# Optimization experiments

Measured on AMD Instinct MI355X. Metric: run time of the kernel, lower is better.

The kernel has to match this reference:

```python
import jax, jax.numpy as jnp
import numpy as np

D_MODEL = 1024
D_STATE = 16
D_CONV = 4
EXPAND = 2
D_INNER = EXPAND * D_MODEL          # 2048
DT_RANK = (D_MODEL + 15) // 16      # 64
EPS = 1e-5
BATCH, SEQ = 2, 1024


def setup_inputs() -> dict:
    key = jax.random.key(0)
    ks = jax.random.split(key, 10)
    s = 0.02
    x = jax.random.normal(ks[0], (BATCH, SEQ, D_MODEL), jnp.float32)
    norm_w = jnp.ones((D_MODEL,), jnp.float32)
    in_proj_w = jax.random.normal(ks[1], (2 * D_INNER, D_MODEL), jnp.float32) * s
    conv_w = jax.random.normal(ks[2], (D_INNER, D_CONV), jnp.float32) * 0.2
    conv_b = jnp.zeros((D_INNER,), jnp.float32)
    x_proj_w = jax.random.normal(ks[3], (DT_RANK + 2 * D_STATE, D_INNER), jnp.float32) * s
    dt_proj_w = jax.random.normal(ks[4], (D_INNER, DT_RANK), jnp.float32) * s
    dt_proj_b = jnp.full((D_INNER,), -2.0, jnp.float32)  # softplus(-2) ~ 0.127, realistic dt init
    # S4D-real init: A[d, n] = n+1  => A_log = log(1..N)
    A_log = jnp.log(jnp.broadcast_to(jnp.arange(1, D_STATE + 1, dtype=jnp.float32), (D_INNER, D_STATE)))
    D = jnp.ones((D_INNER,), jnp.float32)
    out_proj_w = jax.random.normal(ks[5], (D_MODEL, D_INNER), jnp.float32) * s
    return dict(x=x, norm_w=norm_w, in_proj_w=in_proj_w, conv_w=conv_w, conv_b=conv_b,
                x_proj_w=x_proj_w, dt_proj_w=dt_proj_w, dt_proj_b=dt_proj_b,
                A_log=A_log, D=D, out_proj_w=out_proj_w)


def _mamba_forward(x, norm_w, in_proj_w, conv_w, conv_b, x_proj_w,
                   dt_proj_w, dt_proj_b, A_log, D, out_proj_w):
    # Block: residual = x ; h = RMSNorm(residual) ; out = Mamba(h)
    residual = x
    h = x * jax.lax.rsqrt(jnp.mean(x * x, axis=-1, keepdims=True) + EPS) * norm_w

    # in_proj -> split into (xc, z), each [B, L, D_INNER]
    xz = jnp.einsum('bld,ed->ble', h, in_proj_w)
    xc, z = jnp.split(xz, 2, axis=-1)

    # causal depthwise conv1d (kernel D_CONV) + SiLU
    xp = jnp.pad(xc, ((0, 0), (D_CONV - 1, 0), (0, 0)))
    conv = conv_b
    for k in range(D_CONV):  # tiny fixed loop over kernel taps
        conv = conv + conv_w[:, k] * xp[:, k:k + SEQ, :]
    xs = jax.nn.silu(conv)  # [B, L, D_INNER]

    # x_proj -> dt, B_t, C_t
    x_dbl = jnp.einsum('bld,ed->ble', xs, x_proj_w)
    dt_r = x_dbl[..., :DT_RANK]
    B_t = x_dbl[..., DT_RANK:DT_RANK + D_STATE]           # [B, L, N]
    C_t = x_dbl[..., DT_RANK + D_STATE:]                  # [B, L, N]
    dt = jax.nn.softplus(jnp.einsum('blr,dr->bld', dt_r, dt_proj_w) + dt_proj_b)  # [B, L, D_INNER]

    # selective scan: h_t = exp(dt*A) h_{t-1} + dt * B_t * u_t ; y_t = C_t . h_t + D u_t
    A = -jnp.exp(A_log)                                   # [D_INNER, N]
    deltaA = jnp.exp(dt[..., None] * A)                   # [B, L, D_INNER, N]
    deltaBu = (dt * xs)[..., None] * B_t[:, :, None, :]   # [B, L, D_INNER, N]

    def combine(e1, e2):
        a1, b1 = e1
        a2, b2 = e2
        return a1 * a2, a2 * b1 + b2

    _, hstates = jax.lax.associative_scan(combine, (deltaA, deltaBu), axis=1)
    y = jnp.einsum('bldn,bln->bld', hstates, C_t) + D * xs
    y = y * jax.nn.silu(z)
    out = jnp.einsum('bld,ed->ble', y, out_proj_w)

    # MambaBlock: y = mixer_out + residual
    return out + residual


def reference(x, norm_w, in_proj_w, conv_w, conv_b, x_proj_w,
              dt_proj_w, dt_proj_b, A_log, D, out_proj_w):
    return _mamba_forward(x, norm_w, in_proj_w, conv_w, conv_b, x_proj_w,
                          dt_proj_w, dt_proj_b, A_log, D, out_proj_w)
```

## Files before the change

### kernel.cpp

```cpp
#include <hip/hip_runtime.h>
#include <hip/hip_bf16.h>


#define BATCH 2
#define SEQ 1024
#define DMODEL 1024
#define DINNER 2048
#define DTRANK 64
#define DSTATE 16
#define NROWS (BATCH * SEQ)
#define NC 32
#define CL (SEQ / NC)
#define NSPLIT 8
#define KCH (DINNER / NSPLIT)

typedef __bf16 bf16_t;
typedef __bf16 bf16x4 __attribute__((ext_vector_type(4)));
typedef __bf16 bf16x8 __attribute__((ext_vector_type(8)));
typedef float f32x4 __attribute__((ext_vector_type(4)));

__global__ __launch_bounds__(256) void k_prep(
    const float* __restrict__ x, const float* __restrict__ w,
    bf16_t* __restrict__ h,
    const float* __restrict__ s0, bf16_t* __restrict__ d0,
    const float* __restrict__ s1, bf16_t* __restrict__ d1,
    const float* __restrict__ s2, bf16_t* __restrict__ d2)
{
    const int tid = threadIdx.x;
    if (blockIdx.x < NROWS) {
        const int row = blockIdx.x;
        const float* xr = x + (size_t)row * DMODEL;
        float4 xv = *(const float4*)(xr + tid * 4);
        float s = xv.x * xv.x + xv.y * xv.y + xv.z * xv.z + xv.w * xv.w;
#pragma unroll
        for (int m = 1; m <= 32; m <<= 1) s += __shfl_xor(s, m, 64);
        __shared__ float red[4];
        if ((tid & 63) == 0) red[tid >> 6] = s;
        __syncthreads();
        float tot = red[0] + red[1] + red[2] + red[3];
        float scale = rsqrtf(tot * (1.0f / DMODEL) + 1e-5f);
        float4 wv = *(const float4*)(w + tid * 4);
        bf16x4 hv;
        hv.x = (bf16_t)(xv.x * scale * wv.x);
        hv.y = (bf16_t)(xv.y * scale * wv.y);
        hv.z = (bf16_t)(xv.z * scale * wv.z);
        hv.w = (bf16_t)(xv.w * scale * wv.w);
        *(bf16x4*)(h + (size_t)row * DMODEL + tid * 4) = hv;
        return;
    }
    const int i = (blockIdx.x - NROWS) * 256 + tid;
    const float* src; bf16_t* dst; int off;
    if (i < 1048576) { src = s0; dst = d0; off = i; }
    else if (i < 1048576 + 524288) { src = s1; dst = d1; off = i - 1048576; }
    else { src = s2; dst = d2; off = i - 1048576 - 524288; }
    float4 v = *(const float4*)(src + (size_t)off * 4);
    bf16x4 o;
    o.x = (bf16_t)v.x; o.y = (bf16_t)v.y; o.z = (bf16_t)v.z; o.w = (bf16_t)v.w;
    *(bf16x4*)(dst + (size_t)off * 4) = o;
}

template <int BM, int BN, bool BF16_OUT>
__global__ __launch_bounds__(256) void k_gemm_db(
    const bf16_t* __restrict__ A,
    const bf16_t* __restrict__ W,
    void* __restrict__ Cv, int ldc,
    const float* __restrict__ resid,
    int K)
{
    constexpr int NGA = BM / 32;
    constexpr int NGB = BN / 32;
    constexpr int MF = BM / 32;
    constexpr int NF = BN / 32;

    __shared__ __align__(16) bf16_t lA[2][BM * 64];
    __shared__ __align__(16) bf16_t lB[2][BN * 64];

    const int tid = threadIdx.x;
    const int wave = tid >> 6;
    const int lane = tid & 63;
    const int m0 = blockIdx.x * BM;
    const int n0 = blockIdx.y * BN;
    const int wm = (wave >> 1) * (BM / 2);
    const int wn = (wave & 1) * (BN / 2);
    const int fr = lane & 15;
    const int fg = lane >> 4;

    int a_row[NGA], a_col[NGA], b_row[NGB], b_col[NGB];
#pragma unroll
    for (int g = 0; g < NGA; ++g) {
        const int gi = g * 256 + tid;
        a_row[g] = gi >> 3;
        a_col[g] = (gi & 7) ^ (a_row[g] & 7);
    }
#pragma unroll
    for (int g = 0; g < NGB; ++g) {
        const int gi = g * 256 + tid;
        b_row[g] = gi >> 3;
        b_col[g] = (gi & 7) ^ (b_row[g] & 7);
    }

    f32x4 acc[MF][NF] = {};
    bf16x8 ra[NGA], rb[NGB];

#pragma unroll
    for (int g = 0; g < NGA; ++g)
        ra[g] = *(const bf16x8*)(A + (size_t)(m0 + a_row[g]) * K + a_col[g] * 8);
#pragma unroll
    for (int g = 0; g < NGB; ++g)
        rb[g] = *(const bf16x8*)(W + (size_t)(n0 + b_row[g]) * K + b_col[g] * 8);
#pragma unroll
    for (int g = 0; g < NGA; ++g)
        *(bf16x8*)(lA[0] + (size_t)(g * 256 + tid) * 8) = ra[g];
#pragma unroll
    for (int g = 0; g < NGB; ++g)
        *(bf16x8*)(lB[0] + (size_t)(g * 256 + tid) * 8) = rb[g];

    for (int k0 = 0; k0 < K; k0 += 64) {
        const int p = (k0 >> 6) & 1;
        const bool more = (k0 + 64) < K;
        __syncthreads();
        if (more) {
#pragma unroll
            for (int g = 0; g < NGA; ++g)
                ra[g] = *(const bf16x8*)(A + (size_t)(m0 + a_row[g]) * K + (k0 + 64) + a_col[g] * 8);
#pragma unroll
            for (int g = 0; g < NGB; ++g)
                rb[g] = *(const bf16x8*)(W + (size_t)(n0 + b_row[g]) * K + (k0 + 64) + b_col[g] * 8);
        }
#pragma unroll
        for (int s = 0; s < 2; ++s) {
            bf16x8 af[MF], bf[NF];
#pragma unroll
            for (int i = 0; i < MF; ++i) {
                const int rr = wm + i * 16 + fr;
                af[i] = *(const bf16x8*)(lA[p] + (size_t)(rr * 8 + ((s * 4 + fg) ^ (rr & 7))) * 8);
            }
#pragma unroll
            for (int j = 0; j < NF; ++j) {
                const int rr = wn + j * 16 + fr;
                bf[j] = *(const bf16x8*)(lB[p] + (size_t)(rr * 8 + ((s * 4 + fg) ^ (rr & 7))) * 8);
            }
#pragma unroll
            for (int i = 0; i < MF; ++i)
#pragma unroll
                for (int j = 0; j < NF; ++j)
                    acc[i][j] = __builtin_amdgcn_mfma_f32_16x16x32_bf16(
                        af[i], bf[j], acc[i][j], 0, 0, 0);
        }
        if (more) {
#pragma unroll
            for (int g = 0; g < NGA; ++g)
                *(bf16x8*)(lA[p ^ 1] + (size_t)(g * 256 + tid) * 8) = ra[g];
#pragma unroll
            for (int g = 0; g < NGB; ++g)
                *(bf16x8*)(lB[p ^ 1] + (size_t)(g * 256 + tid) * 8) = rb[g];
        }
    }

#pragma unroll
    for (int i = 0; i < MF; ++i) {
        const int rbase = m0 + wm + i * 16 + (lane >> 4) * 4;
#pragma unroll
        for (int rr = 0; rr < 4; ++rr) {
            const int row = rbase + rr;
            if (BF16_OUT) {
                bf16_t* cr = (bf16_t*)Cv + (size_t)row * ldc;
#pragma unroll
                for (int j = 0; j < NF; ++j)
                    cr[n0 + wn + j * 16 + fr] = (bf16_t)acc[i][j][rr];
            } else {
                float* cr = (float*)Cv + (size_t)row * ldc;
                const float* ar = resid + (size_t)row * ldc;
#pragma unroll
                for (int j = 0; j < NF; ++j) {
                    const int col = n0 + wn + j * 16 + fr;
                    cr[col] = acc[i][j][rr] + ar[col];
                }
            }
        }
    }
}

#define XBK 16
__global__ __launch_bounds__(256) void k_gemm_xproj(
    const bf16_t* __restrict__ xz,
    const float* __restrict__ cw,
    const float* __restrict__ cb,
    const float* __restrict__ W,
    float* __restrict__ part,
    bf16_t* __restrict__ xsout)
{
    __shared__ __align__(16) float As[XBK][64 + 4];
    __shared__ __align__(16) float Ws[XBK][96 + 4];
    __shared__ float cwL[KCH * 4];
    __shared__ float cbL[KCH];
    const int tid = threadIdx.x;
    const int m0 = blockIdx.x * 64;
    const int kbase = blockIdx.y * KCH;
    const int lrow = tid >> 2;
    const int lk4 = (tid & 3) << 2;
    const int tm = tid >> 4;
    const int tn = tid & 15;

    {
        float4 v = *(const float4*)(cw + (size_t)kbase * 4 + tid * 4);
        *(float4*)&cwL[tid * 4] = v;
        cbL[tid] = cb[kbase + tid];
    }
    __syncthreads();

    float acc[4][6] = {};

    for (int k0 = 0; k0 < KCH; k0 += XBK) {
        {
            const int eloc = k0 + lk4;
            const int l = m0 + lrow;
            const int lloc = l & (SEQ - 1);
            float s0 = cbL[eloc], s1 = cbL[eloc + 1],
                  s2 = cbL[eloc + 2], s3 = cbL[eloc + 3];
#pragma unroll
            for (int kk = 0; kk < 4; ++kk) {
                const int ll = lloc - 3 + kk;
                if (ll >= 0) {
                    bf16x4 xv = *(const bf16x4*)(xz + (size_t)(l - 3 + kk) * (2 * DINNER)
                                                 + kbase + eloc);
                    s0 = fmaf(cwL[(eloc + 0) * 4 + kk], (float)xv.x, s0);
                    s1 = fmaf(cwL[(eloc + 1) * 4 + kk], (float)xv.y, s1);
                    s2 = fmaf(cwL[(eloc + 2) * 4 + kk], (float)xv.z, s2);
                    s3 = fmaf(cwL[(eloc + 3) * 4 + kk], (float)xv.w, s3);
                }
            }
            s0 = s0 / (1.0f + __expf(-s0));
            s1 = s1 / (1.0f + __expf(-s1));
            s2 = s2 / (1.0f + __expf(-s2));
            s3 = s3 / (1.0f + __expf(-s3));
            As[lk4 + 0][lrow] = s0;
            As[lk4 + 1][lrow] = s1;
            As[lk4 + 2][lrow] = s2;
            As[lk4 + 3][lrow] = s3;
            bf16x4 o;
            o.x = (bf16_t)s0; o.y = (bf16_t)s1; o.z = (bf16_t)s2; o.w = (bf16_t)s3;
            *(bf16x4*)(xsout + (size_t)l * DINNER + kbase + eloc) = o;
        }
        {
            float4 v = *(const float4*)(W + (size_t)lrow * DINNER + kbase + k0 + lk4);
            Ws[lk4 + 0][lrow] = v.x;
            Ws[lk4 + 1][lrow] = v.y;
            Ws[lk4 + 2][lrow] = v.z;
            Ws[lk4 + 3][lrow] = v.w;
        }
        if (tid < 128) {
            float4 v = *(const float4*)(W + (size_t)(64 + lrow) * DINNER + kbase + k0 + lk4);
            Ws[lk4 + 0][64 + lrow] = v.x;
            Ws[lk4 + 1][64 + lrow] = v.y;
            Ws[lk4 + 2][64 + lrow] = v.z;
            Ws[lk4 + 3][64 + lrow] = v.w;
        }
        __syncthreads();
#pragma unroll
        for (int kk = 0; kk < XBK; ++kk) {
            float4 av = *(const float4*)&As[kk][tm * 4];
            float a4[4] = {av.x, av.y, av.z, av.w};
#pragma unroll
            for (int j = 0; j < 6; ++j) {
                const float wv = Ws[kk][tn * 6 + j];
#pragma unroll
                for (int i = 0; i < 4; ++i) acc[i][j] = fmaf(a4[i], wv, acc[i][j]);
            }
        }
        __syncthreads();
    }
    float* pb = part + (size_t)blockIdx.y * NROWS * 96;
#pragma unroll
    for (int i = 0; i < 4; ++i) {
        float* pr = pb + (size_t)(m0 + tm * 4 + i) * 96 + tn * 6;
#pragma unroll
        for (int j = 0; j < 6; ++j) pr[j] = acc[i][j];
    }
}

__global__ __launch_bounds__(256) void k_xproj_reduce(
    const float* __restrict__ part, float* __restrict__ xdbl,
    bf16_t* __restrict__ dtr)
{
    const int idx = blockIdx.x * 256 + threadIdx.x;
    if (idx >= NROWS * 24) return;
    const int row = idx / 24;
    const int c4 = (idx % 24) * 4;
    f32x4 s = {0.f, 0.f, 0.f, 0.f};
#pragma unroll
    for (int p = 0; p < NSPLIT; ++p)
        s += *(const f32x4*)(part + (size_t)p * NROWS * 96 + (size_t)row * 96 + c4);
    *(f32x4*)(xdbl + (size_t)row * 96 + c4) = s;
    if (c4 < 64) {
        bf16x4 o;
        o.x = (bf16_t)s.x; o.y = (bf16_t)s.y; o.z = (bf16_t)s.z; o.w = (bf16_t)s.w;
        *(bf16x4*)(dtr + (size_t)row * 64 + c4) = o;
    }
}

__global__ __launch_bounds__(256) void k_scan_sum(
    const bf16_t* __restrict__ dtlin, const float* __restrict__ dtb,
    const bf16_t* __restrict__ xs, const float* __restrict__ xdbl,
    float* __restrict__ Qpb, float* __restrict__ sloc)
{
    const int tid = threadIdx.x;
    const int g = blockIdx.x & 7;
    const int c = (blockIdx.x >> 3) & (NC - 1);
    const int b = blockIdx.x >> 8;
    const int d0 = g * 256;
    const int d = d0 + tid;

    __shared__ __align__(16) bf16_t sDT[CL * 256];
    __shared__ __align__(16) bf16_t sXS[CL * 256];
    __shared__ float sB[CL * 16];
    {
        const int t = tid >> 4, n = tid & 15;
#pragma unroll
        for (int tt = 0; tt < CL; tt += 16)
            sB[(t + tt) * 16 + n] =
                xdbl[(size_t)(b * SEQ + c * CL + t + tt) * 96 + 64 + n];
    }
#pragma unroll
    for (int i = 0; i < 4; ++i) {
        const int gi = i * 256 + tid;
        const int t = gi >> 5;
        const int c8 = (gi & 31) * 8;
        const size_t ga = (size_t)(b * SEQ + c * CL + t) * DINNER + d0 + c8;
        *(bf16x8*)(sDT + t * 256 + c8) = *(const bf16x8*)(dtlin + ga);
        *(bf16x8*)(sXS + t * 256 + c8) = *(const bf16x8*)(xs + ga);
    }

    float st[16];
#pragma unroll
    for (int n = 0; n < 16; ++n) st[n] = 0.0f;
    float P = 1.0f;
    const float bias = dtb[d];
    __syncthreads();

    for (int t = 0; t < CL; ++t) {
        const float dlv = (float)sDT[t * 256 + tid] + bias;
        const float dtv = (dlv > 20.0f) ? dlv : __logf(1.0f + __expf(dlv));
        const float du = dtv * (float)sXS[t * 256 + tid];
        const float q = __expf(-dtv);
        P *= q;
        float a = q;
#pragma unroll
        for (int n4 = 0; n4 < 4; ++n4) {
            const f32x4 Bv = *(const f32x4*)&sB[t * 16 + n4 * 4];
#pragma unroll
            for (int j = 0; j < 4; ++j) {
                st[n4 * 4 + j] = a * st[n4 * 4 + j] + du * Bv[j];
                a *= q;
            }
        }
    }
    Qpb[(size_t)(b * NC + c) * DINNER + d] = P;
#pragma unroll
    for (int n = 0; n < 16; ++n)
        sloc[((size_t)((b * NC + c) * 16 + n)) * DINNER + d] = st[n];
}

__global__ __launch_bounds__(256) void k_scan_combine(
    const float* __restrict__ Qpb, const float* __restrict__ sloc,
    float* __restrict__ hinit)
{
    const int tid = threadIdx.x;
    const int g = blockIdx.x & 7;
    const int n = (blockIdx.x >> 3) & 15;
    const int b = blockIdx.x >> 7;
    const int d = g * 256 + tid;
    float h = 0.0f;
    for (int c = 0; c < NC; ++c) {
        const size_t i16 = ((size_t)((b * NC + c) * 16 + n)) * DINNER + d;
        hinit[i16] = h;
        const float Q = Qpb[(size_t)(b * NC + c) * DINNER + d];
        float Qn = Q;
        for (int i = 0; i < n; ++i) Qn *= Q;
        h = Qn * h + sloc[i16];
    }
}

__global__ __launch_bounds__(256) void k_scan_out(
    const bf16_t* __restrict__ dtlin, const float* __restrict__ dtb,
    const bf16_t* __restrict__ xs, const float* __restrict__ xdbl,
    const bf16_t* __restrict__ xz, const float* __restrict__ Dp,
    const float* __restrict__ hinit,
    bf16_t* __restrict__ yg)
{
    const int tid = threadIdx.x;
    const int g = blockIdx.x & 7;
    const int c = (blockIdx.x >> 3) & (NC - 1);
    const int b = blockIdx.x >> 8;
    const int d0 = g * 256;
    const int d = d0 + tid;

    __shared__ __align__(16) bf16_t sDT[CL * 256];
    __shared__ __align__(16) bf16_t sXS[CL * 256];
    __shared__ __align__(16) bf16_t sZ[CL * 256];
    __shared__ float sB[CL * 16];
    __shared__ float sC[CL * 16];
    {
        const int t = tid >> 4, n = tid & 15;
#pragma unroll
        for (int tt = 0; tt < CL; tt += 16) {
            const size_t base = (size_t)(b * SEQ + c * CL + t + tt) * 96;
            sB[(t + tt) * 16 + n] = xdbl[base + 64 + n];
            sC[(t + tt) * 16 + n] = xdbl[base + 80 + n];
        }
    }
#pragma unroll
    for (int i = 0; i < 4; ++i) {
        const int gi = i * 256 + tid;
        const int t = gi >> 5;
        const int c8 = (gi & 31) * 8;
        const int row = b * SEQ + c * CL + t;
        const size_t ga = (size_t)row * DINNER + d0 + c8;
        *(bf16x8*)(sDT + t * 256 + c8) = *(const bf16x8*)(dtlin + ga);
        *(bf16x8*)(sXS + t * 256 + c8) = *(const bf16x8*)(xs + ga);
        *(bf16x8*)(sZ + t * 256 + c8) =
            *(const bf16x8*)(xz + (size_t)row * (2 * DINNER) + DINNER + d0 + c8);
    }

    float st[16];
#pragma unroll
    for (int n = 0; n < 16; ++n)
        st[n] = hinit[((size_t)((b * NC + c) * 16 + n)) * DINNER + d];
    const float bias = dtb[d];
    const float Dd = Dp[d];
    __syncthreads();

    for (int t = 0; t < CL; ++t) {
        const float dlv = (float)sDT[t * 256 + tid] + bias;
        const float dtv = (dlv > 20.0f) ? dlv : __logf(1.0f + __expf(dlv));
        const float xv = (float)sXS[t * 256 + tid];
        const float du = dtv * xv;
        const float q = __expf(-dtv);
        float a = q;
        float part = 0.0f;
#pragma unroll
        for (int n4 = 0; n4 < 4; ++n4) {
            const f32x4 Bv = *(const f32x4*)&sB[t * 16 + n4 * 4];
            const f32x4 Cw = *(const f32x4*)&sC[t * 16 + n4 * 4];
#pragma unroll
            for (int j = 0; j < 4; ++j) {
                const int n = n4 * 4 + j;
                st[n] = a * st[n] + du * Bv[j];
                part = fmaf(st[n], Cw[j], part);
                a *= q;
            }
        }
        const float zv = (float)sZ[t * 256 + tid];
        const float sig = 1.0f / (1.0f + __expf(-zv));
        yg[(size_t)(b * SEQ + c * CL + t) * DINNER + d] =
            (bf16_t)((part + Dd * xv) * (zv * sig));
    }
}

extern "C" void kernel_launch(void* const* d_in, const int* in_sizes, int n_in,
                              void* d_out, int out_size, void* d_ws, size_t ws_size,
                              hipStream_t stream) {
    const float* x = (const float*)d_in[0];
    const float* norm_w = (const float*)d_in[1];
    const float* in_proj_w = (const float*)d_in[2];
    const float* conv_w = (const float*)d_in[3];
    const float* conv_b = (const float*)d_in[4];
    const float* x_proj_w = (const float*)d_in[5];
    const float* dt_proj_w = (const float*)d_in[6];
    const float* dt_proj_b = (const float*)d_in[7];
    const float* Dp = (const float*)d_in[9];
    const float* out_proj_w = (const float*)d_in[10];
    float* out = (float*)d_out;

    char* ws = (char*)d_ws;
    bf16_t* xz    = (bf16_t*)(ws);
    bf16_t* xsb   = (bf16_t*)(ws + 16777216);
    float*  xdbl  = (float*) (ws + 25165824);
    bf16_t* dtl   = (bf16_t*)(ws + 25952256);
    float*  sloc  = (float*) (ws + 34340864);
    float*  Qpb   = (float*) (ws + 42729472);
    float*  hinit = (float*) (ws + 43253760);
    bf16_t* ygb   = (bf16_t*)(ws + 51642368);
    bf16_t* hb    = (bf16_t*)(ws + 60030976);
    bf16_t* inw   = (bf16_t*)(ws + 64225280);
    bf16_t* outw  = (bf16_t*)(ws + 72613888);
    bf16_t* dtw   = (bf16_t*)(ws + 76808192);
    bf16_t* dtr   = (bf16_t*)(ws + 77070336);
    float*  xpart = (float*) (ws + 77332480);

    k_prep<<<NROWS + 6272, 256, 0, stream>>>(x, norm_w, hb,
                                             in_proj_w, inw,
                                             out_proj_w, outw,
                                             dt_proj_w, dtw);

    {
        dim3 g(NROWS / 128, (2 * DINNER) / 128);
        k_gemm_db<128, 128, true><<<g, 256, 0, stream>>>(hb, inw, xz, 2 * DINNER,
                                                         nullptr, DMODEL);
    }

    {
        dim3 g(NROWS / 64, NSPLIT);
        k_gemm_xproj<<<g, 256, 0, stream>>>(xz, conv_w, conv_b, x_proj_w,
                                            xpart, xsb);
    }
    k_xproj_reduce<<<(NROWS * 24 + 255) / 256, 256, 0, stream>>>(xpart, xdbl, dtr);

    {
        dim3 g(NROWS / 64, DINNER / 128);
        k_gemm_db<64, 128, true><<<g, 256, 0, stream>>>(dtr, dtw, dtl, DINNER,
                                                        nullptr, DTRANK);
    }

    k_scan_sum<<<BATCH * NC * 8, 256, 0, stream>>>(dtl, dt_proj_b, xsb, xdbl,
                                                   Qpb, sloc);
    k_scan_combine<<<BATCH * DSTATE * 8, 256, 0, stream>>>(Qpb, sloc, hinit);
    k_scan_out<<<BATCH * NC * 8, 256, 0, stream>>>(dtl, dt_proj_b, xsb, xdbl,
                                                   xz, Dp, hinit, ygb);

    {
        dim3 g(NROWS / 64, DMODEL / 64);
        k_gemm_db<64, 64, false><<<g, 256, 0, stream>>>(ygb, outw, out, DMODEL,
                                                        x, DINNER);
    }
}
```

Baseline: 238.5 us.

## Double-buffer xproj GEMM shared tiles and halve row tile to 32

The fused conv+SiLU+x_proj GEMM now uses a 32-row tile instead of 64, doubling the grid, and double-buffers the A/W shared-memory tiles. Global loads for the next K step are issued before the current step's FMAs and written to the alternate buffer afterwards, so one barrier per step is dropped. Each thread now computes a 2x6 accumulator with vectorized float2 LDS reads. The aim is more parallelism and latency hiding, at the cost of more redundant W loads across blocks and lower arithmetic intensity per thread.

```diff
diff --git a/kernel.cpp b/kernel.cpp
--- a/kernel.cpp
+++ b/kernel.cpp
@@ -15,6 +15,7 @@
 #define KCH (DINNER / NSPLIT)
 
 typedef __bf16 bf16_t;
+typedef __bf16 bf16x2 __attribute__((ext_vector_type(2)));
 typedef __bf16 bf16x4 __attribute__((ext_vector_type(4)));
 typedef __bf16 bf16x8 __attribute__((ext_vector_type(8)));
 typedef float f32x4 __attribute__((ext_vector_type(4)));
@@ -190,90 +191,116 @@
     float* __restrict__ part,
     bf16_t* __restrict__ xsout)
 {
-    __shared__ __align__(16) float As[XBK][64 + 4];
-    __shared__ __align__(16) float Ws[XBK][96 + 4];
+    __shared__ __align__(16) float As[2][XBK][36];
+    __shared__ __align__(16) float Ws[2][XBK][100];
     __shared__ float cwL[KCH * 4];
     __shared__ float cbL[KCH];
     const int tid = threadIdx.x;
-    const int m0 = blockIdx.x * 64;
+    const int m0 = blockIdx.x * 32;
     const int kbase = blockIdx.y * KCH;
-    const int lrow = tid >> 2;
-    const int lk4 = (tid & 3) << 2;
+
+    const int ar = tid >> 3;
+    const int ac = (tid & 7) << 1;
+    const int wr = tid >> 2;
+    const int wk = (tid & 3) << 2;
     const int tm = tid >> 4;
     const int tn = tid & 15;
+
+    const int l = m0 + ar;
+    const int lloc = l & (SEQ - 1);
 
     {
         float4 v = *(const float4*)(cw + (size_t)kbase * 4 + tid * 4);
         *(float4*)&cwL[tid * 4] = v;
         cbL[tid] = cb[kbase + tid];
     }
+
+    auto stage_load = [&](int kq, bf16x2 (&xv)[4], float4& wv0, float4& wv1) {
+#pragma unroll
+        for (int kk = 0; kk < 4; ++kk) {
+            bf16x2 z = {};
+            xv[kk] = z;
+            if (lloc - 3 + kk >= 0)
+                xv[kk] = *(const bf16x2*)(xz + (size_t)(l - 3 + kk) * (2 * DINNER)
+                                          + kbase + kq + ac);
+        }
+        wv0 = *(const float4*)(W + (size_t)wr * DINNER + kbase + kq + wk);
+        if (tid < 128)
+            wv1 = *(const float4*)(W + (size_t)(64 + wr) * DINNER + kbase + kq + wk);
+    };
+
+    auto stage_write = [&](int kq, int pbuf, const bf16x2 (&xv)[4],
+                           const float4& wv0, const float4& wv1) {
+        const int e = kq + ac;
+        float s0 = cbL[e], s1 = cbL[e + 1];
+#pragma unroll
+        for (int kk = 0; kk < 4; ++kk) {
+            s0 = fmaf(cwL[(e + 0) * 4 + kk], (float)xv[kk].x, s0);
+            s1 = fmaf(cwL[(e + 1) * 4 + kk], (float)xv[kk].y, s1);
+        }
+        s0 = s0 / (1.0f + __expf(-s0));
+        s1 = s1 / (1.0f + __expf(-s1));
+        As[pbuf][ac + 0][ar] = s0;
+        As[pbuf][ac + 1][ar] = s1;
+        bf16x2 o;
+        o.x = (bf16_t)s0; o.y = (bf16_t)s1;
+        *(bf16x2*)(xsout + (size_t)l * DINNER + kbase + e) = o;
+        Ws[pbuf][wk + 0][wr] = wv0.x;
+        Ws[pbuf][wk + 1][wr] = wv0.y;
+        Ws[pbuf][wk + 2][wr] = wv0.z;
+        Ws[pbuf][wk + 3][wr] = wv0.w;
+        if (tid < 128) {
+            Ws[pbuf][wk + 0][64 + wr] = wv1.x;
+            Ws[pbuf][wk + 1][64 + wr] = wv1.y;
+            Ws[pbuf][wk + 2][64 + wr] = wv1.z;
+            Ws[pbuf][wk + 3][64 + wr] = wv1.w;
+        }
+    };
+
     __syncthreads();
 
-    float acc[4][6] = {};
-
-    for (int k0 = 0; k0 < KCH; k0 += XBK) {
-        {
-            const int eloc = k0 + lk4;
-            const int l = m0 + lrow;
-            const int lloc = l & (SEQ - 1);
-            float s0 = cbL[eloc], s1 = cbL[eloc + 1],
-                  s2 = cbL[eloc + 2], s3 = cbL[eloc + 3];
-#pragma unroll
-            for (int kk = 0; kk < 4; ++kk) {
-                const int ll = lloc - 3 + kk;
-                if (ll >= 0) {
-                    bf16x4 xv = *(const bf16x4*)(xz + (size_t)(l - 3 + kk) * (2 * DINNER)
-                                                 + kbase + eloc);
-                    s0 = fmaf(cwL[(eloc + 0) * 4 + kk], (float)xv.x, s0);
-                    s1 = fmaf(cwL[(eloc + 1) * 4 + kk], (float)xv.y, s1);
-                    s2 = fmaf(cwL[(eloc + 2) * 4 + kk], (float)xv.z, s2);
-                    s3 = fmaf(cwL[(eloc + 3) * 4 + kk], (float)xv.w, s3);
-                }
-            }
-            s0 = s0 / (1.0f + __expf(-s0));
-            s1 = s1 / (1.0f + __expf(-s1));
-            s2 = s2 / (1.0f + __expf(-s2));
-            s3 = s3 / (1.0f + __expf(-s3));
-            As[lk4 + 0][lrow] = s0;
-            As[lk4 + 1][lrow] = s1;
-            As[lk4 + 2][lrow] = s2;
-            As[lk4 + 3][lrow] = s3;
-            bf16x4 o;
-            o.x = (bf16_t)s0; o.y = (bf16_t)s1; o.z = (bf16_t)s2; o.w = (bf16_t)s3;
-            *(bf16x4*)(xsout + (size_t)l * DINNER + kbase + eloc) = o;
-        }
-        {
-            float4 v = *(const float4*)(W + (size_t)lrow * DINNER + kbase + k0 + lk4);
-            Ws[lk4 + 0][lrow] = v.x;
-            Ws[lk4 + 1][lrow] = v.y;
-            Ws[lk4 + 2][lrow] = v.z;
-            Ws[lk4 + 3][lrow] = v.w;
-        }
-        if (tid < 128) {
-            float4 v = *(const float4*)(W + (size_t)(64 + lrow) * DINNER + kbase + k0 + lk4);
-            Ws[lk4 + 0][64 + lrow] = v.x;
-            Ws[lk4 + 1][64 + lrow] = v.y;
-            Ws[lk4 + 2][64 + lrow] = v.z;
-            Ws[lk4 + 3][64 + lrow] = v.w;
-        }
+    {
+        bf16x2 xv[4]; float4 wv0 = {}, wv1 = {};
+        stage_load(0, xv, wv0, wv1);
+        stage_write(0, 0, xv, wv0, wv1);
+    }
+
+    float acc[2][6] = {};
+    constexpr int NSTEP = KCH / XBK;
+
+    for (int ks = 0; ks < NSTEP; ++ks) {
+        const int p = ks & 1;
         __syncthreads();
+        const bool more = (ks + 1) < NSTEP;
+        bf16x2 xv[4]; float4 wv0 = {}, wv1 = {};
+        if (more) stage_load((ks + 1) * XBK, xv, wv0, wv1);
+
 #pragma unroll
         for (int kk = 0; kk < XBK; ++kk) {
-            float4 av = *(const float4*)&As[kk][tm * 4];
-            float a4[4] = {av.x, av.y, av.z, av.w};
-#pragma unroll
-            for (int j = 0; j < 6; ++j) {
-                const float wv = Ws[kk][tn * 6 + j];
-#pragma unroll
-                for (int i = 0; i < 4; ++i) acc[i][j] = fmaf(a4[i], wv, acc[i][j]);
-            }
-        }
-        __syncthreads();
-    }
+            const float2 av  = *(const float2*)&As[p][kk][tm * 2];
+            const float2 w01 = *(const float2*)&Ws[p][kk][tn * 6 + 0];
+            const float2 w23 = *(const float2*)&Ws[p][kk][tn * 6 + 2];
+            const float2 w45 = *(const float2*)&Ws[p][kk][tn * 6 + 4];
+            acc[0][0] = fmaf(av.x, w01.x, acc[0][0]);
+            acc[1][0] = fmaf(av.y, w01.x, acc[1][0]);
+            acc[0][1] = fmaf(av.x, w01.y, acc[0][1]);
+            acc[1][1] = fmaf(av.y, w01.y, acc[1][1]);
+            acc[0][2] = fmaf(av.x, w23.x, acc[0][2]);
+            acc[1][2] = fmaf(av.y, w23.x, acc[1][2]);
+            acc[0][3] = fmaf(av.x, w23.y, acc[0][3]);
+            acc[1][3] = fmaf(av.y, w23.y, acc[1][3]);
+            acc[0][4] = fmaf(av.x, w45.x, acc[0][4]);
+            acc[1][4] = fmaf(av.y, w45.x, acc[1][4]);
+            acc[0][5] = fmaf(av.x, w45.y, acc[0][5]);
+            acc[1][5] = fmaf(av.y, w45.y, acc[1][5]);
+        }
+        if (more) stage_write((ks + 1) * XBK, p ^ 1, xv, wv0, wv1);
+    }
+
     float* pb = part + (size_t)blockIdx.y * NROWS * 96;
 #pragma unroll
-    for (int i = 0; i < 4; ++i) {
-        float* pr = pb + (size_t)(m0 + tm * 4 + i) * 96 + tn * 6;
+    for (int i = 0; i < 2; ++i) {
+        float* pr = pb + (size_t)(m0 + tm * 2 + i) * 96 + tn * 6;
 #pragma unroll
         for (int j = 0; j < 6; ++j) pr[j] = acc[i][j];
     }
@@ -500,7 +527,7 @@
     }
 
     {
-        dim3 g(NROWS / 64, NSPLIT);
+        dim3 g(NROWS / 32, NSPLIT);
         k_gemm_xproj<<<g, 256, 0, stream>>>(xz, conv_w, conv_b, x_proj_w,
                                             xpart, xsb);
     }
```

After: 230.6 us. -3.3%, faster.
